# Kernel optimization log

Measured on AMD Instinct MI355X. Metric: run time of the kernel, lower is better.

The kernel has to match this reference:

```python
import jax, jax.numpy as jnp
import numpy as np

DIM = 384
HEADS = 12
WS = (2, 7, 7)
SS = (1, 3, 3)
B, D, H, W = 4, 8, 56, 56
N = WS[0] * WS[1] * WS[2]  # 98


def _win_part_np(x, ws):
    b, d, h, w, c = x.shape
    x = x.reshape(b, d // ws[0], ws[0], h // ws[1], ws[1], w // ws[2], ws[2], c)
    return x.transpose(0, 1, 3, 5, 2, 4, 6, 7).reshape(-1, ws[0] * ws[1] * ws[2], c)


def setup_inputs() -> dict:
    key = jax.random.key(0)
    ks = jax.random.split(key, 6)
    s = 0.02
    x = jax.random.normal(ks[0], (B, D, H, W, DIM), jnp.float32)
    # relative position index (static int buffer)
    coords = np.stack(np.meshgrid(np.arange(WS[0]), np.arange(WS[1]), np.arange(WS[2]), indexing='ij')).reshape(3, -1)
    rel = (coords[:, :, None] - coords[:, None, :]).transpose(1, 2, 0)
    rel[..., 0] += WS[0] - 1
    rel[..., 1] += WS[1] - 1
    rel[..., 2] += WS[2] - 1
    rel[..., 0] *= (2 * WS[1] - 1) * (2 * WS[2] - 1)
    rel[..., 1] *= 2 * WS[2] - 1
    rel_index = jnp.asarray(rel.sum(-1), jnp.int32)  # [N, N]
    # shifted-window attention mask (standard Swin construction)
    img = np.zeros((1, D, H, W, 1), np.float32)
    cnt = 0
    for dsl in (slice(0, -WS[0]), slice(-WS[0], -SS[0]), slice(-SS[0], None)):
        for hsl in (slice(0, -WS[1]), slice(-WS[1], -SS[1]), slice(-SS[1], None)):
            for wsl in (slice(0, -WS[2]), slice(-WS[2], -SS[2]), slice(-SS[2], None)):
                img[:, dsl, hsl, wsl, :] = cnt
                cnt += 1
    mw = _win_part_np(img, WS).squeeze(-1)  # [nW, N]
    attn_mask = np.where(mw[:, None, :] != mw[:, :, None], -100.0, 0.0).astype(np.float32)
    table_size = (2 * WS[0] - 1) * (2 * WS[1] - 1) * (2 * WS[2] - 1)
    return {
        'x': x,
        'mask': jnp.asarray(attn_mask),
        'rel_table': jax.random.normal(ks[1], (table_size, HEADS), jnp.float32) * s,
        'rel_index': rel_index,
        'qkv_w': jax.random.normal(ks[2], (3 * DIM, DIM), jnp.float32) * s,
        'qkv_b': jnp.zeros((3 * DIM,), jnp.float32),
        'proj_w': jax.random.normal(ks[3], (DIM, DIM), jnp.float32) * s,
        'proj_b': jnp.zeros((DIM,), jnp.float32),
        'g1': jnp.ones((DIM,), jnp.float32), 'b1': jnp.zeros((DIM,), jnp.float32),
        'g2': jnp.ones((DIM,), jnp.float32), 'b2': jnp.zeros((DIM,), jnp.float32),
        'fc1_w': jax.random.normal(ks[4], (DIM, DIM), jnp.float32) * s,
        'fc1_b': jnp.zeros((DIM,), jnp.float32),
        'fc2_w': jax.random.normal(ks[5], (DIM, DIM), jnp.float32) * s,
        'fc2_b': jnp.zeros((DIM,), jnp.float32),
    }


def _ln(x, g, b, eps=1e-5):
    mu = x.mean(-1, keepdims=True)
    var = jnp.mean((x - mu) ** 2, axis=-1, keepdims=True)
    return (x - mu) * jax.lax.rsqrt(var + eps) * g + b


def _window_partition(x, ws):
    b, d, h, w, c = x.shape
    x = x.reshape(b, d // ws[0], ws[0], h // ws[1], ws[1], w // ws[2], ws[2], c)
    return x.transpose(0, 1, 3, 5, 2, 4, 6, 7).reshape(-1, ws[0] * ws[1] * ws[2], c)


def _window_reverse(win, ws, b, d, h, w):
    x = win.reshape(b, d // ws[0], h // ws[1], w // ws[2], ws[0], ws[1], ws[2], -1)
    return x.transpose(0, 1, 4, 2, 5, 3, 6, 7).reshape(b, d, h, w, -1)


def reference(x, mask, rel_table, rel_index, qkv_w, qkv_b, proj_w, proj_b,
              g1, b1, g2, b2, fc1_w, fc1_b, fc2_w, fc2_b):
    shortcut = x
    h = _ln(x, g1, b1)
    b, d, hh, ww, c = h.shape
    # get_window_size: clamp window/shift to input extents (static here)
    ws = [min(WS[i], (d, hh, ww)[i]) for i in range(3)]
    ss = [0 if (d, hh, ww)[i] <= WS[i] else SS[i] for i in range(3)]
    pad = [(ws[i] - (d, hh, ww)[i] % ws[i]) % ws[i] for i in range(3)]
    h = jnp.pad(h, ((0, 0), (0, pad[0]), (0, pad[1]), (0, pad[2]), (0, 0)))
    dp, hp, wp = h.shape[1:4]
    if any(ss):
        h = jnp.roll(h, shift=(-ss[0], -ss[1], -ss[2]), axis=(1, 2, 3))
    xw = _window_partition(h, ws)  # [B_, N, C]
    bw, n, _ = xw.shape
    hd = c // HEADS
    qkv = (xw @ qkv_w.T + qkv_b).reshape(bw, n, 3, HEADS, hd).transpose(2, 0, 3, 1, 4)
    q, k, v = qkv[0], qkv[1], qkv[2]  # [B_, H, N, hd]
    scale = hd ** -0.5
    attn = jnp.einsum('bhnd,bhmd->bhnm', q * scale, k)
    bias = rel_table[rel_index[:n, :n].reshape(-1)].reshape(n, n, HEADS).transpose(2, 0, 1)
    attn = attn + bias[None]
    nW = mask.shape[0]
    attn = attn.reshape(bw // nW, nW, HEADS, n, n) + mask[None, :, None]
    attn = jax.nn.softmax(attn.reshape(bw, HEADS, n, n), axis=-1)
    out = jnp.einsum('bhnm,bhmd->bhnd', attn, v).transpose(0, 2, 1, 3).reshape(bw, n, c)
    out = out @ proj_w.T + proj_b
    out = _window_reverse(out, ws, b, dp, hp, wp)
    if any(ss):
        out = jnp.roll(out, shift=(ss[0], ss[1], ss[2]), axis=(1, 2, 3))
    out = out[:, :d, :hh, :ww, :]
    x1 = shortcut + out
    h2 = _ln(x1, g2, b2)
    mlp = jax.nn.gelu(h2 @ fc1_w.T + fc1_b, approximate=False) @ fc2_w.T + fc2_b
    return x1 + mlp
```

## Files before the change

### kernel.cpp

```cpp
#include <hip/hip_runtime.h>
#include <hip/hip_bf16.h>

#define HEADS 12
#define NWIN 1024
#define NW_MASK 256
#define NTOK 98
#define CDIM 384
#define NROWS (NWIN * NTOK)
#define QKVN (3 * CDIM)
#define PSTR 136
#define LOG2E 1.4426950408889634f
#define SCALE_LOG2E 0.25503486f
#define KSTEPS 12

using u16 = unsigned short;
typedef __attribute__((ext_vector_type(8))) short short8;
typedef __attribute__((ext_vector_type(4))) short s16x4;
typedef __attribute__((ext_vector_type(4))) float f32x4;
typedef __attribute__((ext_vector_type(2))) unsigned u32x2;

__device__ __forceinline__ float b2f(u16 u) { return __uint_as_float(((unsigned)u) << 16); }
__device__ __forceinline__ u16 f2b(float f) {
  unsigned u = __float_as_uint(f);
  u += 0x7FFF + ((u >> 16) & 1);
  return (u16)(u >> 16);
}

__device__ __forceinline__ int tok_of_row(int r) {
  int win = r / NTOK;
  int j   = r - win * NTOK;
  int b   = win >> 8;
  int wl  = win & 255;
  int wd = wl >> 6, wh = (wl >> 3) & 7, ww = wl & 7;
  int od = j / 49; int rem = j - od * 49;
  int oh = rem / 7; int ow = rem - oh * 7;
  int sd = (wd * 2 + od + 1) & 7;
  int sh = wh * 7 + oh + 3; if (sh >= 56) sh -= 56;
  int sw = ww * 7 + ow + 3; if (sw >= 56) sw -= 56;
  return ((b * 8 + sd) * 56 + sh) * 56 + sw;
}

__device__ __forceinline__ int xcd_swz(int bid, int nwg) {
  int q = nwg >> 3, r = nwg & 7;
  int xcd = bid & 7, i = bid >> 3;
  return ((xcd < r) ? xcd * (q + 1) : r * (q + 1) + (xcd - r) * q) + i;
}

__global__ void detect_kernel(const unsigned* __restrict__ g1w, int* __restrict__ flag) {
  if (threadIdx.x == 0 && blockIdx.x == 0)
    flag[0] = (g1w[0] == 0x3F800000u) ? 1 : 0;
}

__device__ __forceinline__ float raw_at(const void* src, size_t j, int isf32) {
  return isf32 ? ((const float*)src)[j] : b2f(((const u16*)src)[j]);
}

struct CvtArgs {
  const void* src[12];
  unsigned off[13];
};
__global__ __launch_bounds__(256) void cvt_all(CvtArgs a, u16* __restrict__ dst,
                                               const int* __restrict__ flag) {
  int i = blockIdx.x * 256 + threadIdx.x;
  if (i >= (int)a.off[12]) return;
  int s = 0;
#pragma unroll
  for (int k = 1; k < 12; ++k) s += (i >= (int)a.off[k]);
  int j = i - (int)a.off[s];
  dst[i] = flag[0] ? f2b(((const float*)a.src[s])[j]) : ((const u16*)a.src[s])[j];
}

template<bool GATHER>
__global__ __launch_bounds__(256) void ln_kernel(const void* __restrict__ in,
                                                 const u16* __restrict__ gam,
                                                 const u16* __restrict__ bet,
                                                 u16* __restrict__ outp,
                                                 const int* __restrict__ flag,
                                                 int maybe_f32) {
  int wrow = blockIdx.x * 4 + (threadIdx.x >> 6);
  int lane = threadIdx.x & 63;
  int isf32 = maybe_f32 ? flag[0] : 0;
  size_t srow = GATHER ? (size_t)tok_of_row(wrow) : (size_t)wrow;
  const u16*   ip16 = (const u16*)in + srow * CDIM;
  const float* ip32 = (const float*)in + srow * CDIM;
  float xv[6]; float s = 0.f, s2 = 0.f;
#pragma unroll
  for (int i = 0; i < 6; ++i) {
    int c = lane + 64 * i;
    xv[i] = isf32 ? ip32[c] : b2f(ip16[c]);
    s += xv[i]; s2 += xv[i] * xv[i];
  }
#pragma unroll
  for (int off = 1; off < 64; off <<= 1) {
    s  += __shfl_xor(s, off);
    s2 += __shfl_xor(s2, off);
  }
  float mu = s * (1.f / CDIM);
  float var = s2 * (1.f / CDIM) - mu * mu;
  float rstd = rsqrtf(var + 1e-5f);
  u16* op = outp + (size_t)wrow * CDIM;
#pragma unroll
  for (int i = 0; i < 6; ++i) {
    int c = lane + 64 * i;
    op[c] = f2b((xv[i] - mu) * rstd * b2f(gam[c]) + b2f(bet[c]));
  }
}

__global__ void bias_kernel(const void* __restrict__ tab, const int* __restrict__ idx,
                            float* __restrict__ biasf, const int* __restrict__ flag) {
  int i = blockIdx.x * 256 + threadIdx.x;
  if (i >= HEADS * NTOK * 100) return;
  int isf32 = flag[0];
  int h = i / (NTOK * 100);
  int rem = i - h * (NTOK * 100);
  int q = rem / 100, t = rem - q * 100;
  biasf[i] = (t < NTOK) ? raw_at(tab, (size_t)idx[q * NTOK + t] * HEADS + h, isf32) * LOG2E : 0.f;
}

__global__ void maskp_kernel(const void* __restrict__ msrc, u16* __restrict__ mdst,
                             const int* __restrict__ flag) {
  int i = blockIdx.x * 256 + threadIdx.x;
  if (i >= NW_MASK * NTOK * 100) return;
  int isf32 = flag[0];
  int w = i / (NTOK * 100);
  int rem = i - w * (NTOK * 100);
  int q = rem / 100, t = rem - q * 100;
  mdst[i] = (t < NTOK) ? f2b(raw_at(msrc, (size_t)(w * NTOK + q) * NTOK + t, isf32) * LOG2E)
                       : (u16)0;
}

__device__ __forceinline__ void gload16(const u16* g, u16* l) {
  __builtin_amdgcn_global_load_lds((const __attribute__((address_space(1))) unsigned*)g,
                                   (__attribute__((address_space(3))) unsigned*)l,
                                   16, 0, 0);
}

template<int EPI>
__global__ __launch_bounds__(256) void gemm_bt(const u16* __restrict__ A, int lda,
                                               const u16* __restrict__ W,
                                               const u16* __restrict__ bias,
                                               int NB, void* __restrict__ outb, int ldo,
                                               const void* __restrict__ aux,
                                               const int* __restrict__ flag) {
  __shared__ __align__(16) u16 lA[2][128 * 32];
  __shared__ __align__(16) u16 lB[2][128 * 32];
  int bid = xcd_swz(blockIdx.x, gridDim.x);
  int mb = bid / NB, nb = bid - mb * NB;
  int row0 = mb * 128, col0 = nb * 128;
  int tid = threadIdx.x;
  int lane = tid & 63;
  int wid = tid >> 6;
  int wr = (wid >> 1) * 64, wc = (wid & 1) * 64;
  f32x4 zero = {0.f, 0.f, 0.f, 0.f};
  f32x4 acc[4][4];
#pragma unroll
  for (int m = 0; m < 4; ++m)
#pragma unroll
    for (int n = 0; n < 4; ++n) acc[m][n] = zero;

  int r0 = tid >> 2, s0 = tid & 3;
  int r1 = 64 + r0;
  int c0 = 8 * (s0 ^ ((r0 >> 1) & 3));
  int c1 = 8 * (s0 ^ ((r1 >> 1) & 3));
  const u16* Ab0 = &A[(size_t)(row0 + r0) * lda + c0];
  const u16* Ab1 = &A[(size_t)(row0 + r1) * lda + c1];
  const u16* Wb0 = &W[(size_t)(col0 + r0) * CDIM + c0];
  const u16* Wb1 = &W[(size_t)(col0 + r1) * CDIM + c1];
  int e0 = tid * 8, e1 = 2048 + tid * 8;
  int g = (lane >> 4) * 8, fr = lane & 15;
  int sw = 8 * ((lane >> 4) ^ ((fr >> 1) & 3));

  gload16(Ab0, &lA[0][e0]);
  gload16(Ab1, &lA[0][e1]);
  gload16(Wb0, &lB[0][e0]);
  gload16(Wb1, &lB[0][e1]);
  __syncthreads();

#pragma unroll
  for (int t = 0; t < KSTEPS; ++t) {
    int cur = t & 1;
    if (t < KSTEPS - 1) {
      int kt = (t + 1) * 32;
      gload16(Ab0 + kt, &lA[cur ^ 1][e0]);
      gload16(Ab1 + kt, &lA[cur ^ 1][e1]);
      gload16(Wb0 + kt, &lB[cur ^ 1][e0]);
      gload16(Wb1 + kt, &lB[cur ^ 1][e1]);
    }
    short8 af[4], bf[4];
#pragma unroll
    for (int m = 0; m < 4; ++m) af[m] = *(const short8*)&lA[cur][(wr + m * 16 + fr) * 32 + sw];
#pragma unroll
    for (int n = 0; n < 4; ++n) bf[n] = *(const short8*)&lB[cur][(wc + n * 16 + fr) * 32 + sw];
#pragma unroll
    for (int m = 0; m < 4; ++m)
#pragma unroll
      for (int n = 0; n < 4; ++n)
        acc[m][n] = __builtin_amdgcn_mfma_f32_16x16x32_bf16(af[m], bf[n], acc[m][n], 0, 0, 0);
    __syncthreads();
  }

  int isf32 = (EPI == 1 || EPI == 3) ? flag[0] : 0;
  int colo = lane & 15;
  int rowo = (lane >> 4) * 4;
  float bv[4];
#pragma unroll
  for (int n = 0; n < 4; ++n) bv[n] = b2f(bias[col0 + wc + n * 16 + colo]);
#pragma unroll
  for (int m = 0; m < 4; ++m) {
#pragma unroll
    for (int r = 0; r < 4; ++r) {
      int gr = row0 + wr + m * 16 + rowo + r;
      int t = (EPI == 1 || EPI == 3) ? tok_of_row(gr) : 0;
      int win = 0, tok = 0;
      if (EPI == 0) { win = gr / NTOK; tok = gr - win * NTOK; }
#pragma unroll
      for (int n = 0; n < 4; ++n) {
        int gc = col0 + wc + n * 16 + colo;
        float v = acc[m][n][r] + bv[n];
        if (EPI == 0) {
          int cb = col0 + wc + n * 16;
          int which = cb / 384;
          int rem = cb - which * 384;
          int hh = rem >> 5, dd = rem & 31;
          ((u16*)outb)[((((size_t)win * 3 + which) * HEADS + hh) * NTOK + tok) * 32 + dd + colo] = f2b(v);
        } else if (EPI == 1) {
          float xs = isf32 ? ((const float*)aux)[(size_t)t * CDIM + gc]
                           : b2f(((const u16*)aux)[(size_t)t * CDIM + gc]);
          ((u16*)outb)[(size_t)gr * ldo + gc] = f2b(v + xs);
        } else if (EPI == 2) {
          float ge = 0.5f * v * (1.f + erff(v * 0.70710678118654752f));
          ((u16*)outb)[(size_t)gr * ldo + gc] = f2b(ge);
        } else {
          float x1v = b2f(((const u16*)aux)[(size_t)gr * CDIM + gc]);
          float o = v + x1v;
          if (isf32) ((float*)outb)[(size_t)t * CDIM + gc] = o;
          else       ((u16*)outb)[(size_t)t * CDIM + gc] = f2b(o);
        }
      }
    }
  }
}

__global__ __launch_bounds__(256, 3) void attn_mfma(const u16* __restrict__ qkvB,
                                                    u16* __restrict__ obuf,
                                                    const u16* __restrict__ maskp,
                                                    const float* __restrict__ biasf) {
  __shared__ __align__(16) u16 P4[4][16 * PSTR];
  int wid = threadIdx.x >> 6, lane = threadIdx.x & 63;
  int gh = blockIdx.x * 4 + wid;
  int win = gh / HEADS, hd = gh - win * HEADS;
  int l15 = lane & 15, g = lane >> 4;
  u16* P = P4[wid];
  const size_t hsz = (size_t)NTOK * 32;
  const u16* qp = qkvB + ((size_t)(win * 3 + 0) * HEADS + hd) * hsz;
  const u16* kp = qkvB + ((size_t)(win * 3 + 1) * HEADS + hd) * hsz;
  const u16* vp = qkvB + ((size_t)(win * 3 + 2) * HEADS + hd) * hsz;
  u16* op = obuf + ((size_t)win * NTOK) * CDIM + hd * 32;
  const f32x4 zero = {0.f, 0.f, 0.f, 0.f};

  { u32x2 z = {0u, 0u}; *(u32x2*)&P[l15 * PSTR + 112 + 4 * g] = z; }

  short8 kf[7];
#pragma unroll
  for (int n = 0; n < 7; ++n) {
    int tok = n * 16 + l15; if (tok > NTOK - 1) tok = NTOK - 1;
    kf[n] = *(const short8*)&kp[tok * 32 + 8 * g];
  }
  short8 vf[2][4];
#pragma unroll
  for (int kk = 0; kk < 4; ++kk)
#pragma unroll
    for (int i = 0; i < 8; ++i) {
      int tok = 32 * kk + 8 * g + i;
      const u16* vr = vp + tok * 32 + l15;
      u16 v0 = (tok < NTOK) ? vr[0]  : (u16)0;
      u16 v1 = (tok < NTOK) ? vr[16] : (u16)0;
      vf[0][kk][i] = (short)v0;
      vf[1][kk][i] = (short)v1;
    }

  const float* brow = biasf + (size_t)hd * NTOK * 100;
  const u16*   mrow = maskp + (size_t)(win & (NW_MASK - 1)) * NTOK * 100;

  for (int m = 0; m < 7; ++m) {
    int qrow = m * 16 + l15;
    int qr = qrow > NTOK - 1 ? NTOK - 1 : qrow;
    short8 qf = *(const short8*)&qp[qr * 32 + 8 * g];
    f32x4 st[7];
#pragma unroll
    for (int n = 0; n < 7; ++n)
      st[n] = __builtin_amdgcn_mfma_f32_16x16x32_bf16(kf[n], qf, zero, 0, 0, 0);

    float pv[7][4];
    float mx = -1e30f;
#pragma unroll
    for (int n = 0; n < 7; ++n) {
      f32x4 bb = *(const f32x4*)&brow[(size_t)qr * 100 + n * 16 + 4 * g];
      s16x4 mm = *(const s16x4*)&mrow[(size_t)qr * 100 + n * 16 + 4 * g];
#pragma unroll
      for (int r = 0; r < 4; ++r) {
        int tok = n * 16 + 4 * g + r;
        float s = st[n][r] * SCALE_LOG2E + bb[r] + b2f((u16)mm[r]);
        if (tok > NTOK - 1) s = -1e30f;
        pv[n][r] = s;
        mx = fmaxf(mx, s);
      }
    }
    mx = fmaxf(mx, __shfl_xor(mx, 16));
    mx = fmaxf(mx, __shfl_xor(mx, 32));
    float sum = 0.f;
#pragma unroll
    for (int n = 0; n < 7; ++n)
#pragma unroll
      for (int r = 0; r < 4; ++r) {
        float e = exp2f(pv[n][r] - mx);
        pv[n][r] = e; sum += e;
      }
    sum += __shfl_xor(sum, 16);
    sum += __shfl_xor(sum, 32);
    float inv = 1.f / sum;
#pragma unroll
    for (int n = 0; n < 7; ++n) {
      __hip_bfloat162 h0 = __float22bfloat162_rn(make_float2(pv[n][0] * inv, pv[n][1] * inv));
      __hip_bfloat162 h1 = __float22bfloat162_rn(make_float2(pv[n][2] * inv, pv[n][3] * inv));
      u32x2 wv = { *(unsigned*)&h0, *(unsigned*)&h1 };
      *(u32x2*)&P[l15 * PSTR + n * 16 + 4 * g] = wv;
    }
    f32x4 oa0 = zero, oa1 = zero;
#pragma unroll
    for (int kk = 0; kk < 4; ++kk) {
      short8 pf = *(const short8*)&P[l15 * PSTR + kk * 32 + 8 * g];
      oa0 = __builtin_amdgcn_mfma_f32_16x16x32_bf16(pf, vf[0][kk], oa0, 0, 0, 0);
      oa1 = __builtin_amdgcn_mfma_f32_16x16x32_bf16(pf, vf[1][kk], oa1, 0, 0, 0);
    }
#pragma unroll
    for (int r = 0; r < 4; ++r) {
      int row = m * 16 + 4 * g + r;
      if (row < NTOK) {
        op[(size_t)row * CDIM + l15]      = f2b(oa0[r]);
        op[(size_t)row * CDIM + 16 + l15] = f2b(oa1[r]);
      }
    }
  }
}

extern "C" void kernel_launch(void* const* d_in, const int* in_sizes, int n_in,
                              void* d_out, int out_size, void* d_ws, size_t ws_size,
                              hipStream_t stream) {
  (void)n_in; (void)out_size; (void)ws_size;
  const void* x    = d_in[0];
  const int* ridx  = (const int*)d_in[3];

  char* ws = (char*)d_ws;
  const size_t SZ_QKV = (size_t)NROWS * QKVN * 2;
  const size_t SZ_MAT = (size_t)NROWS * CDIM * 2;
  const size_t SZ_BIAS = (size_t)HEADS * NTOK * 100 * 4;
  const size_t SZ_MASKP = (size_t)NW_MASK * NTOK * 100 * 2;
  u16* qkvB    = (u16*)ws;
  u16* bufA    = (u16*)(ws + SZ_QKV);
  u16* bufX1   = (u16*)(ws + SZ_QKV + SZ_MAT);
  float* biasf = (float*)(ws + SZ_QKV + 2 * SZ_MAT);
  u16* maskp   = (u16*)(ws + SZ_QKV + 2 * SZ_MAT + SZ_BIAS);
  int* flag    = (int*)(ws + SZ_QKV + 2 * SZ_MAT + SZ_BIAS + SZ_MASKP);
  u16* cvt     = (u16*)((char*)flag + 256);

  detect_kernel<<<1, 64, 0, stream>>>((const unsigned*)d_in[8], flag);

  CvtArgs ca;
  unsigned off = 0;
  u16* cp[16];
  for (int k = 0; k < 12; ++k) {
    int i = 4 + k;
    ca.src[k] = d_in[i];
    ca.off[k] = off;
    cp[i] = cvt + off;
    off += (unsigned)in_sizes[i];
  }
  ca.off[12] = off;
  cvt_all<<<(off + 255) / 256, 256, 0, stream>>>(ca, cvt, flag);

  bias_kernel<<<(HEADS * NTOK * 100 + 255) / 256, 256, 0, stream>>>(d_in[2], ridx, biasf, flag);
  maskp_kernel<<<(NW_MASK * NTOK * 100 + 255) / 256, 256, 0, stream>>>(d_in[1], maskp, flag);
  ln_kernel<true><<<NROWS / 4, 256, 0, stream>>>(x, cp[8], cp[9], bufA, flag, 1);
  gemm_bt<0><<<(NROWS / 128) * (QKVN / 128), 256, 0, stream>>>(
      bufA, CDIM, cp[4], cp[5], QKVN / 128, qkvB, 0, nullptr, flag);
  attn_mfma<<<(NWIN * HEADS) / 4, 256, 0, stream>>>(qkvB, bufA, maskp, biasf);
  gemm_bt<1><<<(NROWS / 128) * (CDIM / 128), 256, 0, stream>>>(
      bufA, CDIM, cp[6], cp[7], CDIM / 128, bufX1, CDIM, x, flag);
  ln_kernel<false><<<NROWS / 4, 256, 0, stream>>>(bufX1, cp[10], cp[11], bufA, flag, 0);
  u16* fc1out = qkvB;
  gemm_bt<2><<<(NROWS / 128) * (CDIM / 128), 256, 0, stream>>>(
      bufA, CDIM, cp[12], cp[13], CDIM / 128, fc1out, CDIM, nullptr, flag);
  gemm_bt<3><<<(NROWS / 128) * (CDIM / 128), 256, 0, stream>>>(
      fc1out, CDIM, cp[14], cp[15], CDIM / 128, d_out, CDIM, bufX1, flag);
}
```

Baseline: 848.7 us.

## Fuse LayerNorm, FC1+GELU and FC2+residual into one MLP kernel

Replaces the separate LN2 kernel and two GEMM launches with a single kernel that normalizes a 128-row tile into LDS, runs FC1 with GELU back into LDS, then runs FC2 and adds the residual. This removes the global round-trips for the normalized activations and the FC1 output, plus two launches. In exchange it uses about 147 KB of LDS per block with 512 threads and holds a large register footprint, which may limit occupancy, and it streams the full weight matrices per row tile.

```diff
diff --git a/kernel.cpp b/kernel.cpp
--- a/kernel.cpp
+++ b/kernel.cpp
@@ -12,6 +12,8 @@
 #define LOG2E 1.4426950408889634f
 #define SCALE_LOG2E 0.25503486f
 #define KSTEPS 12
+#define MBLK 128
+#define XN_STR 392
 
 using u16 = unsigned short;
 typedef __attribute__((ext_vector_type(8))) short short8;
@@ -199,7 +201,7 @@
     __syncthreads();
   }
 
-  int isf32 = (EPI == 1 || EPI == 3) ? flag[0] : 0;
+  int isf32 = (EPI == 1) ? flag[0] : 0;
   int colo = lane & 15;
   int rowo = (lane >> 4) * 4;
   float bv[4];
@@ -210,7 +212,7 @@
 #pragma unroll
     for (int r = 0; r < 4; ++r) {
       int gr = row0 + wr + m * 16 + rowo + r;
-      int t = (EPI == 1 || EPI == 3) ? tok_of_row(gr) : 0;
+      int t = (EPI == 1) ? tok_of_row(gr) : 0;
       int win = 0, tok = 0;
       if (EPI == 0) { win = gr / NTOK; tok = gr - win * NTOK; }
 #pragma unroll
@@ -223,18 +225,10 @@
           int rem = cb - which * 384;
           int hh = rem >> 5, dd = rem & 31;
           ((u16*)outb)[((((size_t)win * 3 + which) * HEADS + hh) * NTOK + tok) * 32 + dd + colo] = f2b(v);
-        } else if (EPI == 1) {
+        } else {
           float xs = isf32 ? ((const float*)aux)[(size_t)t * CDIM + gc]
                            : b2f(((const u16*)aux)[(size_t)t * CDIM + gc]);
           ((u16*)outb)[(size_t)gr * ldo + gc] = f2b(v + xs);
-        } else if (EPI == 2) {
-          float ge = 0.5f * v * (1.f + erff(v * 0.70710678118654752f));
-          ((u16*)outb)[(size_t)gr * ldo + gc] = f2b(ge);
-        } else {
-          float x1v = b2f(((const u16*)aux)[(size_t)gr * CDIM + gc]);
-          float o = v + x1v;
-          if (isf32) ((float*)outb)[(size_t)t * CDIM + gc] = o;
-          else       ((u16*)outb)[(size_t)t * CDIM + gc] = f2b(o);
         }
       }
     }
@@ -344,6 +338,151 @@
   }
 }
 
+__global__ __launch_bounds__(512, 2) void mlp_fused(const u16* __restrict__ x1,
+                                                    const u16* __restrict__ gam,
+                                                    const u16* __restrict__ bet,
+                                                    const u16* __restrict__ w1,
+                                                    const u16* __restrict__ b1v,
+                                                    const u16* __restrict__ w2,
+                                                    const u16* __restrict__ b2v,
+                                                    void* __restrict__ outp,
+                                                    const int* __restrict__ flag) {
+  __shared__ __align__(16) u16 xn[MBLK * XN_STR];
+  __shared__ __align__(16) u16 bt[2][384 * 32];
+  int tid = threadIdx.x, lane = tid & 63, wid = tid >> 6;
+  int l15 = lane & 15, g = lane >> 4;
+  int rgrp = wid >> 1, cgrp = wid & 1;
+  int row0 = blockIdx.x * MBLK;
+  const f32x4 zero = {0.f, 0.f, 0.f, 0.f};
+
+  {
+    int row = tid >> 2, q = tid & 3;
+    const u16* ip = x1 + (size_t)(row0 + row) * CDIM + q * 96;
+    short8 xv[12]; float s = 0.f, s2 = 0.f;
+#pragma unroll
+    for (int i = 0; i < 12; ++i) {
+      xv[i] = *(const short8*)&ip[i * 8];
+#pragma unroll
+      for (int e = 0; e < 8; ++e) { float f = b2f((u16)xv[i][e]); s += f; s2 += f * f; }
+    }
+    s += __shfl_xor(s, 1); s2 += __shfl_xor(s2, 1);
+    s += __shfl_xor(s, 2); s2 += __shfl_xor(s2, 2);
+    float mu = s * (1.f / CDIM);
+    float var = s2 * (1.f / CDIM) - mu * mu;
+    float rstd = rsqrtf(var + 1e-5f);
+    u16* op = &xn[row * XN_STR + q * 96];
+#pragma unroll
+    for (int i = 0; i < 12; ++i) {
+      short8 o;
+#pragma unroll
+      for (int e = 0; e < 8; ++e) {
+        int c = q * 96 + i * 8 + e;
+        o[e] = (short)f2b((b2f((u16)xv[i][e]) - mu) * rstd * b2f(gam[c]) + b2f(bet[c]));
+      }
+      *(short8*)&op[i * 8] = o;
+    }
+  }
+  __syncthreads();
+
+  short8 af[2][KSTEPS];
+#pragma unroll
+  for (int m = 0; m < 2; ++m)
+#pragma unroll
+    for (int kk = 0; kk < KSTEPS; ++kk)
+      af[m][kk] = *(const short8*)&xn[(rgrp * 32 + m * 16 + l15) * XN_STR + kk * 32 + 8 * g];
+
+#define STAGE_B(W, kk, buf)                                             \
+  {                                                                     \
+    _Pragma("unroll")                                                   \
+    for (int i = 0; i < 3; ++i) {                                       \
+      int j = i * 512 + tid;                                            \
+      int c = j >> 2, q = j & 3;                                        \
+      gload16(&(W)[(size_t)c * CDIM + (kk) * 32 + 8 * (q ^ (c & 3))],   \
+              &bt[buf][j * 8]);                                         \
+    }                                                                   \
+  }
+
+  f32x4 acc[2][12];
+#pragma unroll
+  for (int m = 0; m < 2; ++m)
+#pragma unroll
+    for (int n = 0; n < 12; ++n) acc[m][n] = zero;
+
+  STAGE_B(w1, 0, 0);
+  __syncthreads();
+#pragma unroll
+  for (int kk = 0; kk < KSTEPS; ++kk) {
+    int cur = kk & 1;
+    if (kk < KSTEPS - 1) STAGE_B(w1, kk + 1, cur ^ 1);
+#pragma unroll
+    for (int n = 0; n < 12; ++n) {
+      int c = cgrp * 192 + n * 16 + l15;
+      short8 bf = *(const short8*)&bt[cur][c * 32 + 8 * (g ^ (l15 & 3))];
+#pragma unroll
+      for (int m = 0; m < 2; ++m)
+        acc[m][n] = __builtin_amdgcn_mfma_f32_16x16x32_bf16(af[m][kk], bf, acc[m][n], 0, 0, 0);
+    }
+    __syncthreads();
+  }
+
+#pragma unroll
+  for (int m = 0; m < 2; ++m)
+#pragma unroll
+    for (int n = 0; n < 12; ++n) {
+      int c = cgrp * 192 + n * 16 + l15;
+      float bb = b2f(b1v[c]);
+#pragma unroll
+      for (int r = 0; r < 4; ++r) {
+        float v = acc[m][n][r] + bb;
+        float ge = 0.5f * v * (1.f + erff(v * 0.70710678118654752f));
+        xn[(rgrp * 32 + m * 16 + 4 * g + r) * XN_STR + c] = f2b(ge);
+        acc[m][n][r] = 0.f;
+      }
+    }
+  __syncthreads();
+
+#pragma unroll
+  for (int m = 0; m < 2; ++m)
+#pragma unroll
+    for (int kk = 0; kk < KSTEPS; ++kk)
+      af[m][kk] = *(const short8*)&xn[(rgrp * 32 + m * 16 + l15) * XN_STR + kk * 32 + 8 * g];
+
+  STAGE_B(w2, 0, 0);
+  __syncthreads();
+#pragma unroll
+  for (int kk = 0; kk < KSTEPS; ++kk) {
+    int cur = kk & 1;
+    if (kk < KSTEPS - 1) STAGE_B(w2, kk + 1, cur ^ 1);
+#pragma unroll
+    for (int n = 0; n < 12; ++n) {
+      int c = cgrp * 192 + n * 16 + l15;
+      short8 bf = *(const short8*)&bt[cur][c * 32 + 8 * (g ^ (l15 & 3))];
+#pragma unroll
+      for (int m = 0; m < 2; ++m)
+        acc[m][n] = __builtin_amdgcn_mfma_f32_16x16x32_bf16(af[m][kk], bf, acc[m][n], 0, 0, 0);
+    }
+    __syncthreads();
+  }
+
+  int isf32 = flag[0];
+#pragma unroll
+  for (int m = 0; m < 2; ++m)
+#pragma unroll
+    for (int r = 0; r < 4; ++r) {
+      int grow = row0 + rgrp * 32 + m * 16 + 4 * g + r;
+      int t = tok_of_row(grow);
+#pragma unroll
+      for (int n = 0; n < 12; ++n) {
+        int c = cgrp * 192 + n * 16 + l15;
+        float v = acc[m][n][r] + b2f(b2v[c]);
+        float o = v + b2f(x1[(size_t)grow * CDIM + c]);
+        if (isf32) ((float*)outp)[(size_t)t * CDIM + c] = o;
+        else       ((u16*)outp)[(size_t)t * CDIM + c] = f2b(o);
+      }
+    }
+#undef STAGE_B
+}
+
 extern "C" void kernel_launch(void* const* d_in, const int* in_sizes, int n_in,
                               void* d_out, int out_size, void* d_ws, size_t ws_size,
                               hipStream_t stream) {
@@ -387,10 +526,6 @@
   attn_mfma<<<(NWIN * HEADS) / 4, 256, 0, stream>>>(qkvB, bufA, maskp, biasf);
   gemm_bt<1><<<(NROWS / 128) * (CDIM / 128), 256, 0, stream>>>(
       bufA, CDIM, cp[6], cp[7], CDIM / 128, bufX1, CDIM, x, flag);
-  ln_kernel<false><<<NROWS / 4, 256, 0, stream>>>(bufX1, cp[10], cp[11], bufA, flag, 0);
-  u16* fc1out = qkvB;
-  gemm_bt<2><<<(NROWS / 128) * (CDIM / 128), 256, 0, stream>>>(
-      bufA, CDIM, cp[12], cp[13], CDIM / 128, fc1out, CDIM, nullptr, flag);
-  gemm_bt<3><<<(NROWS / 128) * (CDIM / 128), 256, 0, stream>>>(
-      fc1out, CDIM, cp[14], cp[15], CDIM / 128, d_out, CDIM, bufX1, flag);
-}
+  mlp_fused<<<NROWS / MBLK, 512, 0, stream>>>(
+      bufX1, cp[10], cp[11], cp[12], cp[13], cp[14], cp[15], d_out, flag);
+}
```

Result: slower. 896.5 us (+5.6%).
